# Optimization experiments

Hardware: AMD Instinct MI355X
Metric: run time of the kernel (lower is better)

Reference implementation:

```python
import jax, jax.numpy as jnp
import numpy as np
import math

B, S, D, H = 2, 2048, 1024, 16
DH = D // H
NEG = -1e9


def gelu(x):
    return 0.5 * x * (1.0 + jnp.tanh(math.sqrt(2.0 / math.pi) * (x + 0.044715 * x ** 3)))


def layernorm(x, g, b, eps=1e-6):
    # faithful to module: uses std (unbiased, N-1) and adds eps to std, not var
    mean = jnp.mean(x, axis=-1, keepdims=True)
    var = jnp.sum((x - mean) ** 2, axis=-1, keepdims=True) / (x.shape[-1] - 1)
    std = jnp.sqrt(var)
    return g * (x - mean) / (std + eps) + b


def setup_inputs() -> dict:
    key = jax.random.key(0)
    ks = jax.random.split(key, 13)
    sd = 0.02
    return {
        "x": jax.random.normal(ks[0], (B, S, D), jnp.float32),
        "w_attn": jax.random.normal(ks[1], (D, 3 * D), jnp.float32) * sd,
        "b_attn": jnp.zeros((3 * D,), jnp.float32),
        "w_aproj": jax.random.normal(ks[2], (D, D), jnp.float32) * sd,
        "b_aproj": jnp.zeros((D,), jnp.float32),
        "g1": jnp.ones((D,), jnp.float32),
        "b1": jnp.zeros((D,), jnp.float32),
        "w_fc": jax.random.normal(ks[3], (D, 4 * D), jnp.float32) * sd,
        "b_fc": jnp.zeros((4 * D,), jnp.float32),
        "w_mproj": jax.random.normal(ks[4], (4 * D, D), jnp.float32) * sd,
        "b_mproj": jnp.zeros((D,), jnp.float32),
        "g2": jnp.ones((D,), jnp.float32),
        "b2": jnp.zeros((D,), jnp.float32),
    }


def reference(x, w_attn, b_attn, w_aproj, b_aproj, g1, b1, w_fc, b_fc, w_mproj, b_mproj, g2, b2):
    # --- attention ---
    qkv = x @ w_attn + b_attn                       # [B,S,3D]
    q, k, v = jnp.split(qkv, 3, axis=2)
    q = q.reshape(B, S, H, DH).transpose(0, 2, 1, 3)  # [B,H,S,DH]
    k = k.reshape(B, S, H, DH).transpose(0, 2, 1, 3)
    v = v.reshape(B, S, H, DH).transpose(0, 2, 1, 3)
    w = jnp.einsum('bhqd,bhkd->bhqk', q, k) / math.sqrt(DH)
    mask = jnp.tril(jnp.ones((S, S), jnp.float32))[None, None]
    w = w * mask + NEG * (1.0 - mask)
    w = jax.nn.softmax(w, axis=-1)
    a = jnp.einsum('bhqk,bhkd->bhqd', w, v)         # [B,H,S,DH]
    a = a.transpose(0, 2, 1, 3).reshape(B, S, D)
    a = a @ w_aproj + b_aproj
    # --- postLN + MLP ---
    n = layernorm(x + a, g1, b1)
    h = gelu(n @ w_fc + b_fc)
    m = h @ w_mproj + b_mproj
    return layernorm(n + m, g2, b2)
```

## Files before the change

### kernel.cpp

```cpp
#include <hip/hip_runtime.h>
#include <type_traits>


typedef unsigned short u16;
typedef short s16x8 __attribute__((ext_vector_type(8)));
typedef unsigned short u16x4 __attribute__((ext_vector_type(4)));
typedef float f32x4 __attribute__((ext_vector_type(4)));
typedef float f32x16 __attribute__((ext_vector_type(16)));

__device__ __forceinline__ u16 f2b(float f) {
    union { float f; unsigned u; } x{f};
    unsigned r = x.u + 0x7FFFu + ((x.u >> 16) & 1u);
    return (u16)(r >> 16);
}

__device__ __forceinline__ float b2f(u16 v) {
    union { unsigned u; float f; } x;
    x.u = ((unsigned)v) << 16;
    return x.f;
}

__device__ __forceinline__ f32x4 mfma16(s16x8 a, s16x8 b, f32x4 c) {
    return __builtin_amdgcn_mfma_f32_16x16x32_bf16(a, b, c, 0, 0, 0);
}

__device__ __forceinline__ f32x16 mfma32(s16x8 a, s16x8 b, f32x16 c) {
    return __builtin_amdgcn_mfma_f32_32x32x16_bf16(a, b, c, 0, 0, 0);
}

__device__ __forceinline__ int cvtpk(float a, float b) {
    int r;
    asm("v_cvt_pk_bf16_f32 %0, %1, %2" : "=v"(r) : "v"(a), "v"(b));
    return r;
}

__device__ __forceinline__ void gld_lds16(const u16* g, const u16* l) {
    __builtin_amdgcn_global_load_lds(
        (const __attribute__((address_space(1))) void*)g,
        (__attribute__((address_space(3))) void*)l, 16, 0, 0);
}

__device__ __forceinline__ void hard_barrier() {
    __builtin_amdgcn_sched_barrier(0);
    __builtin_amdgcn_s_barrier();
    __builtin_amdgcn_sched_barrier(0);
}

__global__ __launch_bounds__(256) void cvt_bf16(const float* __restrict__ in,
                                                u16* __restrict__ out, int n4) {
    int i = blockIdx.x * 256 + threadIdx.x;
    if (i < n4) {
        float4 v = ((const float4*)in)[i];
        u16x4 o = {f2b(v.x), f2b(v.y), f2b(v.z), f2b(v.w)};
        ((u16x4*)out)[i] = o;
    }
}

__global__ __launch_bounds__(256) void transpose_bf16(const float* __restrict__ W,
                                                      u16* __restrict__ WT,
                                                      int K, int N) {
    __shared__ float t[32][33];
    int tx = threadIdx.x & 31, ty = threadIdx.x >> 5;
    int n0 = blockIdx.x * 32, k0 = blockIdx.y * 32;
    #pragma unroll
    for (int r = ty; r < 32; r += 8)
        t[r][tx] = W[(size_t)(k0 + r) * N + n0 + tx];
    __syncthreads();
    #pragma unroll
    for (int r = ty; r < 32; r += 8)
        WT[(size_t)(n0 + r) * K + k0 + tx] = f2b(t[tx][r]);
}

template<int BN, bool GELU, typename OT>
__global__ __launch_bounds__(256) void gemm_pl(const u16* __restrict__ A,
                                               const u16* __restrict__ BT,
                                               const float* __restrict__ bias,
                                               OT* __restrict__ C,
                                               int M, int N, int K, int ldc) {
    constexpr int NF = BN / 32;
    constexpr int BNI = BN / 32;
    constexpr int LTOT = 4 + BNI;
    __shared__ u16 As[2][128 * 64];
    __shared__ u16 Bs[2][BN * 64];

    int t = threadIdx.x;
    int w = t >> 6, l = t & 63, l16 = l & 15, lh = l >> 4;
    int wr = w >> 1, wc = w & 1;

    int nbm = M >> 7;
    int cpx = gridDim.x >> 3;
    int id = blockIdx.x;
    int id2 = (id & 7) * cpx + (id >> 3);
    size_t m0 = (size_t)(id2 % nbm) * 128;
    size_t n0 = (size_t)(id2 / nbm) * BN;

    int rowA = t >> 3;
    int gc2 = (t & 7) ^ (rowA & 7);
    const u16* Ag = A + (m0 + rowA) * (size_t)K + gc2 * 8;
    const u16* Bg = BT + (n0 + rowA) * (size_t)K + gc2 * 8;
    int wbase = w * 512;

    f32x4 acc[4][NF] = {};
    int rx = (l16 & 7) * 8;

    const s16x8* pa[2][4];
    const s16x8* pb[2][NF];
    #pragma unroll
    for (int ks = 0; ks < 2; ++ks) {
        #pragma unroll
        for (int fm = 0; fm < 4; ++fm) {
            int row = wr * 64 + fm * 16 + l16;
            int col = ((ks * 4 + lh) * 8) ^ rx;
            pa[ks][fm] = (const s16x8*)&As[0][row * 64 + col];
        }
        #pragma unroll
        for (int fn = 0; fn < NF; ++fn) {
            int row = wc * (BN / 2) + fn * 16 + l16;
            int col = ((ks * 4 + lh) * 8) ^ rx;
            pb[ks][fn] = (const s16x8*)&Bs[0][row * 64 + col];
        }
    }
    const u16* dA[4];
    const u16* dB[BNI];
    #pragma unroll
    for (int j = 0; j < 4; ++j) dA[j] = &As[0][j * 2048 + wbase];
    #pragma unroll
    for (int j = 0; j < BNI; ++j) dB[j] = &Bs[0][j * 2048 + wbase];

    #pragma unroll
    for (int j = 0; j < 4; ++j) gld_lds16(Ag + (size_t)j * 32 * K, dA[j]);
    #pragma unroll
    for (int j = 0; j < BNI; ++j) gld_lds16(Bg + (size_t)j * 32 * K, dB[j]);
    #pragma unroll
    for (int j = 0; j < 4; ++j)
        gld_lds16(Ag + 64 + (size_t)j * 32 * K, dA[j] + 8192);
    #pragma unroll
    for (int j = 0; j < BNI; ++j)
        gld_lds16(Bg + 64 + (size_t)j * 32 * K, dB[j] + BN * 64);

#define GTILE(CB, kk, LAST)                                                   \
    {                                                                         \
        if (LAST) asm volatile("s_waitcnt vmcnt(0)" ::: "memory");            \
        else      asm volatile("s_waitcnt vmcnt(%0)" :: "n"(LTOT) : "memory");\
        hard_barrier();                                                       \
        __builtin_amdgcn_s_setprio(1);                                        \
        _Pragma("unroll")                                                     \
        for (int ks = 0; ks < 2; ++ks) {                                      \
            s16x8 af[4], bf[NF];                                              \
            _Pragma("unroll")                                                 \
            for (int fm = 0; fm < 4; ++fm) af[fm] = pa[ks][fm][(CB) * 1024];  \
            _Pragma("unroll")                                                 \
            for (int fn = 0; fn < NF; ++fn) bf[fn] = pb[ks][fn][(CB) * BN * 8];\
            _Pragma("unroll")                                                 \
            for (int fm = 0; fm < 4; ++fm)                                    \
                _Pragma("unroll")                                             \
                for (int fn = 0; fn < NF; ++fn)                               \
                    acc[fm][fn] = mfma16(af[fm], bf[fn], acc[fm][fn]);        \
        }                                                                     \
        __builtin_amdgcn_s_setprio(0);                                        \
        hard_barrier();                                                       \
        if ((kk) + 128 < K) {                                                 \
            const u16* Ap = Ag + (kk) + 128;                                  \
            _Pragma("unroll")                                                 \
            for (int j = 0; j < 4; ++j)                                       \
                gld_lds16(Ap + (size_t)j * 32 * K, dA[j] + (CB) * 8192);      \
            const u16* Bp = Bg + (kk) + 128;                                  \
            _Pragma("unroll")                                                 \
            for (int j = 0; j < BNI; ++j)                                     \
                gld_lds16(Bp + (size_t)j * 32 * K, dB[j] + (CB) * (BN * 64)); \
        }                                                                     \
    }

    for (int k0 = 0; k0 < K; k0 += 128) {
        GTILE(0, k0, (k0 + 64 >= K))
        GTILE(1, k0 + 64, (k0 + 128 >= K))
    }
#undef GTILE

    #pragma unroll
    for (int fn = 0; fn < NF; ++fn) {
        size_t col = n0 + wc * (BN / 2) + fn * 16 + l16;
        float bs = bias[col];
        #pragma unroll
        for (int fm = 0; fm < 4; ++fm) {
            size_t row0 = m0 + wr * 64 + fm * 16 + lh * 4;
            #pragma unroll
            for (int i = 0; i < 4; ++i) {
                float v = acc[fm][fn][i] + bs;
                if constexpr (GELU) {
                    float x3 = v * v * v;
                    v = 0.5f * v * (1.f + tanhf(0.7978845608f * (v + 0.044715f * x3)));
                }
                if constexpr (std::is_same<OT, u16>::value)
                    C[(row0 + i) * ldc + col] = f2b(v);
                else
                    C[(row0 + i) * ldc + col] = v;
            }
        }
    }
}

__global__ __launch_bounds__(256) void attn_kernel(const u16* __restrict__ qkv,
                                                   u16* __restrict__ p0,
                                                   u16* __restrict__ p1,
                                                   u16* __restrict__ p2,
                                                   u16* __restrict__ p3,
                                                   float2* __restrict__ stats) {
    constexpr int S = 2048, D3 = 3072, Dm = 1024;
    __shared__ u16 Kl[2][64 * 64];
    __shared__ u16 Vt[2][64 * 64];

    int t = threadIdx.x;
    int w = t >> 6, l = t & 63;
    int l32 = l & 31, hi = l >> 5;
    int bid = blockIdx.x;
    int bh = bid & 31;
    int pr = (bid >> 5) & 7;
    int quar = bid >> 8;
    int b = bh >> 4, h = bh & 15;
    size_t base = (size_t)b * S * D3;

    u16* pout = quar == 0 ? p0 : (quar == 1 ? p1 : (quar == 2 ? p2 : p3));

    int rK0 = t >> 3, gK = t & 7;
    int rK1 = rK0 + 32;
    size_t koff0 = (size_t)rK0 * D3 + (size_t)((gK ^ (rK0 & 7)) * 8);
    size_t koff1 = (size_t)rK1 * D3 + (size_t)((gK ^ (rK1 & 7)) * 8);
    const u16* kbase = qkv + base + Dm + h * 64;
    const u16* vbase = qkv + base + 2 * Dm + h * 64 + w * 16;

    constexpr float cexp = 0.18033688011112042f;
    constexpr float THR = 64.0f;
    int xg = l32 & 7;

    #pragma unroll 1
    for (int ph = 0; ph < 2; ++ph) {
        int qt = ph ? (15 - pr) : pr;
        int qb = qt * 128 + w * 32;
        int nst = 2 * (qt + 1);
        int c0 = (nst * quar) >> 2;
        int c1 = (nst * (quar + 1)) >> 2;

        f32x16 O0 = {}, O1 = {};
        float m = -1e30f, lr = 0.f;

        if (c0 < c1) {
            s16x8 qf[4];
            const u16* qp = qkv + base + (size_t)(qb + l32) * D3 + h * 64 + hi * 8;
            #pragma unroll
            for (int kk = 0; kk < 4; ++kk)
                qf[kk] = *(const s16x8*)(qp + kk * 16);

            size_t kc0 = (size_t)c0 * 64 * D3;
            gld_lds16(kbase + kc0 + koff0, &Kl[0][w * 512]);
            gld_lds16(kbase + kc0 + koff1, &Kl[0][2048 + w * 512]);
            {
                const u16* vp = vbase + (size_t)(c0 * 64 + l) * D3;
                s16x8 pv0 = *(const s16x8*)vp;
                s16x8 pv1 = *(const s16x8*)(vp + 8);
                #pragma unroll
                for (int e = 0; e < 8; ++e) {
                    int d0 = w * 16 + e, d1 = w * 16 + 8 + e;
                    Vt[0][d0 * 64 + (l ^ ((d0 & 7) << 3))] = (u16)pv0[e];
                    Vt[0][d1 * 64 + (l ^ ((d1 & 7) << 3))] = (u16)pv1[e];
                }
            }
            __syncthreads();

            #pragma unroll 1
            for (int sc = c0; sc < c1; ++sc) {
                int cur = (sc - c0) & 1;
                bool pre = (sc + 1 < c1);
                s16x8 v0, v1;
                if (pre) {
                    size_t koffc = (size_t)(sc + 1) * 64 * D3;
                    gld_lds16(kbase + koffc + koff0, &Kl[cur ^ 1][w * 512]);
                    gld_lds16(kbase + koffc + koff1, &Kl[cur ^ 1][2048 + w * 512]);
                    const u16* vp = vbase + (size_t)((sc + 1) * 64 + l) * D3;
                    v0 = *(const s16x8*)vp;
                    v1 = *(const s16x8*)(vp + 8);
                }

                int kvb = sc * 64;
                int navail = ((qb - kvb) >> 5) + 1;
                if (navail > 0) {
                    if (navail > 2) navail = 2;
                    const u16* Kc = Kl[cur];
                    const u16* Vc = Vt[cur];
                    f32x16 sa0 = {}, sa1 = {};
                    #pragma unroll
                    for (int kk = 0; kk < 4; ++kk) {
                        s16x8 kf = *(const s16x8*)&Kc[l32 * 64 + (((2 * kk + hi) ^ xg) * 8)];
                        sa0 = mfma32(kf, qf[kk], sa0);
                    }
                    if (navail == 2) {
                        #pragma unroll
                        for (int kk = 0; kk < 4; ++kk) {
                            s16x8 kf = *(const s16x8*)&Kc[(32 + l32) * 64 + (((2 * kk + hi) ^ xg) * 8)];
                            sa1 = mfma32(kf, qf[kk], sa1);
                        }
                    }
                    bool diag0 = (kvb == qb);
                    bool diag1 = (kvb + 32 == qb);
                    float p[32];
                    float mx = -1e30f;
                    #pragma unroll
                    for (int reg = 0; reg < 16; ++reg) {
                        int kvloc = (reg & 3) + 8 * (reg >> 2) + 4 * hi;
                        float s0 = sa0[reg];
                        if (diag0 && kvloc > l32) s0 = -1e30f;
                        p[reg] = s0;
                        mx = fmaxf(mx, s0);
                    }
                    if (navail == 2) {
                        #pragma unroll
                        for (int reg = 0; reg < 16; ++reg) {
                            int kvloc = (reg & 3) + 8 * (reg >> 2) + 4 * hi;
                            float s1 = sa1[reg];
                            if (diag1 && kvloc > l32) s1 = -1e30f;
                            p[16 + reg] = s1;
                            mx = fmaxf(mx, s1);
                        }
                    }
                    mx = fmaxf(mx, __shfl_xor(mx, 32));
                    if (!__all(mx <= m + THR)) {
                        float mn = fmaxf(m, mx);
                        float a_ = exp2f(cexp * (m - mn));
                        m = mn;
                        #pragma unroll
                        for (int reg = 0; reg < 16; ++reg) {
                            int src = (reg & 3) + 8 * (reg >> 2) + 4 * hi;
                            float aq = __shfl(a_, src);
                            O0[reg] *= aq;
                            O1[reg] *= aq;
                        }
                        lr *= a_;
                    }
                    float cm = cexp * m;
                    float rs = 0.f;
                    #pragma unroll
                    for (int reg = 0; reg < 16; ++reg) {
                        p[reg] = exp2f(fmaf(cexp, p[reg], -cm));
                        rs += p[reg];
                    }
                    if (navail == 2) {
                        #pragma unroll
                        for (int reg = 16; reg < 32; ++reg) {
                            p[reg] = exp2f(fmaf(cexp, p[reg], -cm));
                            rs += p[reg];
                        }
                    }
                    rs += __shfl_xor(rs, 32);
                    lr += rs;

                    #pragma unroll
                    for (int c = 0; c < 4; ++c) {
                        if (c < navail * 2) {
                            int pb = (c >> 1) * 16 + (c & 1) * 8;
                            int pk01 = cvtpk(p[pb + 0], p[pb + 1]);
                            int pk23 = cvtpk(p[pb + 2], p[pb + 3]);
                            int pk45 = cvtpk(p[pb + 4], p[pb + 5]);
                            int pk67 = cvtpk(p[pb + 6], p[pb + 7]);
                            int sx01 = __shfl_xor(pk01, 32);
                            int sx23 = __shfl_xor(pk23, 32);
                            int sx45 = __shfl_xor(pk45, 32);
                            int sx67 = __shfl_xor(pk67, 32);
                            union { int i[4]; s16x8 v; } u;
                            u.i[0] = hi ? sx45 : pk01;
                            u.i[1] = hi ? sx67 : pk23;
                            u.i[2] = hi ? pk45 : sx01;
                            u.i[3] = hi ? pk67 : sx23;
                            int go = ((c * 2 + hi) ^ xg) * 8;
                            s16x8 vb0 = *(const s16x8*)&Vc[l32 * 64 + go];
                            O0 = mfma32(u.v, vb0, O0);
                            s16x8 vb1 = *(const s16x8*)&Vc[(32 + l32) * 64 + go];
                            O1 = mfma32(u.v, vb1, O1);
                        }
                    }
                }

                if (pre) {
                    #pragma unroll
                    for (int e = 0; e < 8; ++e) {
                        int d0 = w * 16 + e, d1 = w * 16 + 8 + e;
                        Vt[cur ^ 1][d0 * 64 + (l ^ ((d0 & 7) << 3))] = (u16)v0[e];
                        Vt[cur ^ 1][d1 * 64 + (l ^ ((d1 & 7) << 3))] = (u16)v1[e];
                    }
                }
                __syncthreads();
            }
        }

        size_t obase = (size_t)b * S * 1024 + h * 64;
        #pragma unroll
        for (int reg = 0; reg < 16; ++reg) {
            int src = (reg & 3) + 8 * (reg >> 2) + 4 * hi;
            size_t row = obase + (size_t)(qb + src) * 1024;
            pout[row + l32] = f2b(O0[reg]);
            pout[row + 32 + l32] = f2b(O1[reg]);
        }
        if (hi == 0) {
            float2 st; st.x = m; st.y = lr;
            stats[quar * 65536 + ((b * 2048 + qb + l32) * 16 + h)] = st;
        }
    }
}

__global__ __launch_bounds__(256) void merge_attn(u16* __restrict__ p0,
                                                  const u16* __restrict__ p1,
                                                  const u16* __restrict__ p2,
                                                  const u16* __restrict__ p3,
                                                  const float2* __restrict__ stats) {
    constexpr float cexp = 0.18033688011112042f;
    int gid = blockIdx.x * 256 + threadIdx.x;
    int rh = gid >> 2;
    int dc = (gid & 3) * 16;
    int R = rh >> 4, h = rh & 15;
    size_t addr = (size_t)R * 1024 + h * 64 + dc;

    float2 s0 = stats[rh];
    float2 s1 = stats[65536 + rh];
    float2 s2 = stats[131072 + rh];
    float2 s3 = stats[196608 + rh];
    float M = fmaxf(fmaxf(s0.x, s1.x), fmaxf(s2.x, s3.x));
    float a0 = exp2f(cexp * (s0.x - M));
    float a1 = exp2f(cexp * (s1.x - M));
    float a2 = exp2f(cexp * (s2.x - M));
    float a3 = exp2f(cexp * (s3.x - M));
    float inv = 1.f / (a0 * s0.y + a1 * s1.y + a2 * s2.y + a3 * s3.y);
    a0 *= inv; a1 *= inv; a2 *= inv; a3 *= inv;

    u16x4 o[4];
    #pragma unroll
    for (int j = 0; j < 4; ++j) {
        u16x4 q0 = *(const u16x4*)(p0 + addr + j * 4);
        u16x4 q1 = *(const u16x4*)(p1 + addr + j * 4);
        u16x4 q2 = *(const u16x4*)(p2 + addr + j * 4);
        u16x4 q3 = *(const u16x4*)(p3 + addr + j * 4);
        #pragma unroll
        for (int e = 0; e < 4; ++e)
            o[j][e] = f2b(a0 * b2f(q0[e]) + a1 * b2f(q1[e]) +
                          a2 * b2f(q2[e]) + a3 * b2f(q3[e]));
    }
    #pragma unroll
    for (int j = 0; j < 4; ++j)
        *(u16x4*)(p0 + addr + j * 4) = o[j];
}

template<bool WB>
__global__ __launch_bounds__(256) void resln(const float* __restrict__ xa,
                                             const float* __restrict__ xb2,
                                             const float* __restrict__ g,
                                             const float* __restrict__ be,
                                             float* __restrict__ outf,
                                             u16* __restrict__ outb) {
    int row = blockIdx.x;
    int t = threadIdx.x;
    size_t base = (size_t)row * 1024 + t * 4;
    float4 va = *(const float4*)(xa + base);
    float4 vb = *(const float4*)(xb2 + base);
    float v0 = va.x + vb.x, v1 = va.y + vb.y, v2 = va.z + vb.z, v3 = va.w + vb.w;
    float s1 = v0 + v1 + v2 + v3;
    float s2 = v0 * v0 + v1 * v1 + v2 * v2 + v3 * v3;
    #pragma unroll
    for (int off = 32; off >= 1; off >>= 1) {
        s1 += __shfl_down(s1, off);
        s2 += __shfl_down(s2, off);
    }
    __shared__ float r1[4], r2[4];
    if ((t & 63) == 0) { r1[t >> 6] = s1; r2[t >> 6] = s2; }
    __syncthreads();
    s1 = r1[0] + r1[1] + r1[2] + r1[3];
    s2 = r2[0] + r2[1] + r2[2] + r2[3];
    float mean = s1 * (1.f / 1024.f);
    float var = fmaxf((s2 - 1024.f * mean * mean) * (1.f / 1023.f), 0.f);
    float inv = 1.f / (sqrtf(var) + 1e-6f);
    int col = t * 4;
    float y0 = g[col + 0] * ((v0 - mean) * inv) + be[col + 0];
    float y1 = g[col + 1] * ((v1 - mean) * inv) + be[col + 1];
    float y2 = g[col + 2] * ((v2 - mean) * inv) + be[col + 2];
    float y3 = g[col + 3] * ((v3 - mean) * inv) + be[col + 3];
    float4 o = {y0, y1, y2, y3};
    *(float4*)(outf + base) = o;
    if constexpr (WB) {
        u16x4 ob = {f2b(y0), f2b(y1), f2b(y2), f2b(y3)};
        *(u16x4*)(outb + base) = ob;
    }
}

extern "C" void kernel_launch(void* const* d_in, const int* in_sizes, int n_in,
                              void* d_out, int out_size, void* d_ws, size_t ws_size,
                              hipStream_t stream) {
    (void)in_sizes; (void)n_in; (void)out_size; (void)ws_size;
    const float* x       = (const float*)d_in[0];
    const float* w_attn  = (const float*)d_in[1];
    const float* b_attn  = (const float*)d_in[2];
    const float* w_aproj = (const float*)d_in[3];
    const float* b_aproj = (const float*)d_in[4];
    const float* g1      = (const float*)d_in[5];
    const float* b1      = (const float*)d_in[6];
    const float* w_fc    = (const float*)d_in[7];
    const float* b_fc    = (const float*)d_in[8];
    const float* w_mproj = (const float*)d_in[9];
    const float* b_mproj = (const float*)d_in[10];
    const float* g2      = (const float*)d_in[11];
    const float* b2      = (const float*)d_in[12];
    float* out = (float*)d_out;

    constexpr int M = 4096;
    constexpr int D = 1024;

    char* ws = (char*)d_ws;
    u16*   slotA = (u16*)ws;
    char*  pB    = ws + (32u << 20);
    char*  pC    = ws + (40u << 20);
    char*  pD    = ws + (48u << 20);
    char*  pE    = ws + (64u << 20);

    u16*   xb    = (u16*)pB;
    u16*   wT    = (u16*)pC;
    u16*   qkv   = slotA;
    u16*   part0 = (u16*)pB;
    u16*   part1 = (u16*)pC;
    u16*   part2 = (u16*)pD;
    u16*   part3 = (u16*)(pD + (8u << 20));
    float2* stat = (float2*)pE;
    u16*   abuf  = (u16*)pB;
    float* aout  = (float*)pD;
    float* nbuf  = (float*)pE;
    u16*   nb    = (u16*)pB;
    u16*   h     = slotA;
    float* mout  = (float*)pD;

    dim3 blk(256);

    cvt_bf16<<<dim3(4096), blk, 0, stream>>>(x, xb, M * D / 4);

    transpose_bf16<<<dim3(3072 / 32, 1024 / 32), blk, 0, stream>>>(w_attn, wT, 1024, 3072);
    gemm_pl<128, false, u16><<<dim3((M / 128) * (3072 / 128)), blk, 0, stream>>>(
        xb, wT, b_attn, qkv, M, 3072, 1024, 3072);

    attn_kernel<<<dim3(1024), blk, 0, stream>>>(qkv, part0, part1, part2, part3, stat);
    merge_attn<<<dim3(1024), blk, 0, stream>>>(part0, part1, part2, part3, stat);

    transpose_bf16<<<dim3(1024 / 32, 1024 / 32), blk, 0, stream>>>(w_aproj, wT, 1024, 1024);
    gemm_pl<64, false, float><<<dim3((M / 128) * (1024 / 64)), blk, 0, stream>>>(
        abuf, wT, b_aproj, aout, M, 1024, 1024, 1024);

    resln<true><<<dim3(M), blk, 0, stream>>>(x, aout, g1, b1, nbuf, nb);

    transpose_bf16<<<dim3(4096 / 32, 1024 / 32), blk, 0, stream>>>(w_fc, wT, 1024, 4096);
    gemm_pl<128, true, u16><<<dim3((M / 128) * (4096 / 128)), blk, 0, stream>>>(
        nb, wT, b_fc, h, M, 4096, 1024, 4096);

    transpose_bf16<<<dim3(1024 / 32, 4096 / 32), blk, 0, stream>>>(w_mproj, wT, 4096, 1024);
    gemm_pl<64, false, float><<<dim3((M / 128) * (1024 / 64)), blk, 0, stream>>>(
        h, wT, b_mproj, mout, M, 1024, 4096, 1024);

    resln<false><<<dim3(M), blk, 0, stream>>>(nbuf, mout, g2, b2, out, nullptr);
}
```

Measured before the change: 286.3 us.

## Use 512-thread GEMM blocks with 2x4 wave grid

Doubles the GEMM workgroup to 8 waves, arranged 2x4, so each wave computes a narrower 64 x BN/4 sub-tile. The global-to-LDS copy is redistributed across 512 threads, and LDS fragment addresses are now computed inline instead of from precomputed pointer arrays. The aim is more resident waves to hide memory and MFMA latency. The cost is less register-level reuse per wave, more LDS reads per MFMA, and heavier block barriers.

```diff
diff --git a/kernel.cpp b/kernel.cpp
--- a/kernel.cpp
+++ b/kernel.cpp
@@ -72,20 +72,20 @@
 }
 
 template<int BN, bool GELU, typename OT>
-__global__ __launch_bounds__(256) void gemm_pl(const u16* __restrict__ A,
+__global__ __launch_bounds__(512) void gemm_pl(const u16* __restrict__ A,
                                                const u16* __restrict__ BT,
                                                const float* __restrict__ bias,
                                                OT* __restrict__ C,
                                                int M, int N, int K, int ldc) {
-    constexpr int NF = BN / 32;
-    constexpr int BNI = BN / 32;
-    constexpr int LTOT = 4 + BNI;
+    constexpr int NF = BN / 64;
+    constexpr int BNI = BN / 64;
+    constexpr int LTOT = 2 + BNI;
     __shared__ u16 As[2][128 * 64];
     __shared__ u16 Bs[2][BN * 64];
 
     int t = threadIdx.x;
     int w = t >> 6, l = t & 63, l16 = l & 15, lh = l >> 4;
-    int wr = w >> 1, wc = w & 1;
+    int wr = w >> 2, wc = w & 3;
 
     int nbm = M >> 7;
     int cpx = gridDim.x >> 3;
@@ -98,45 +98,23 @@
     int gc2 = (t & 7) ^ (rowA & 7);
     const u16* Ag = A + (m0 + rowA) * (size_t)K + gc2 * 8;
     const u16* Bg = BT + (n0 + rowA) * (size_t)K + gc2 * 8;
-    int wbase = w * 512;
+    int wb = w * 512;
 
     f32x4 acc[4][NF] = {};
     int rx = (l16 & 7) * 8;
 
-    const s16x8* pa[2][4];
-    const s16x8* pb[2][NF];
-    #pragma unroll
-    for (int ks = 0; ks < 2; ++ks) {
-        #pragma unroll
-        for (int fm = 0; fm < 4; ++fm) {
-            int row = wr * 64 + fm * 16 + l16;
-            int col = ((ks * 4 + lh) * 8) ^ rx;
-            pa[ks][fm] = (const s16x8*)&As[0][row * 64 + col];
-        }
-        #pragma unroll
-        for (int fn = 0; fn < NF; ++fn) {
-            int row = wc * (BN / 2) + fn * 16 + l16;
-            int col = ((ks * 4 + lh) * 8) ^ rx;
-            pb[ks][fn] = (const s16x8*)&Bs[0][row * 64 + col];
-        }
-    }
-    const u16* dA[4];
-    const u16* dB[BNI];
-    #pragma unroll
-    for (int j = 0; j < 4; ++j) dA[j] = &As[0][j * 2048 + wbase];
-    #pragma unroll
-    for (int j = 0; j < BNI; ++j) dB[j] = &Bs[0][j * 2048 + wbase];
-
-    #pragma unroll
-    for (int j = 0; j < 4; ++j) gld_lds16(Ag + (size_t)j * 32 * K, dA[j]);
-    #pragma unroll
-    for (int j = 0; j < BNI; ++j) gld_lds16(Bg + (size_t)j * 32 * K, dB[j]);
-    #pragma unroll
-    for (int j = 0; j < 4; ++j)
-        gld_lds16(Ag + 64 + (size_t)j * 32 * K, dA[j] + 8192);
+    #pragma unroll
+    for (int j = 0; j < 2; ++j)
+        gld_lds16(Ag + (size_t)j * 64 * K, &As[0][j * 4096 + wb]);
     #pragma unroll
     for (int j = 0; j < BNI; ++j)
-        gld_lds16(Bg + 64 + (size_t)j * 32 * K, dB[j] + BN * 64);
+        gld_lds16(Bg + (size_t)j * 64 * K, &Bs[0][j * 4096 + wb]);
+    #pragma unroll
+    for (int j = 0; j < 2; ++j)
+        gld_lds16(Ag + 64 + (size_t)j * 64 * K, &As[1][j * 4096 + wb]);
+    #pragma unroll
+    for (int j = 0; j < BNI; ++j)
+        gld_lds16(Bg + 64 + (size_t)j * 64 * K, &Bs[1][j * 4096 + wb]);
 
 #define GTILE(CB, kk, LAST)                                                   \
     {                                                                         \
@@ -148,9 +126,17 @@
         for (int ks = 0; ks < 2; ++ks) {                                      \
             s16x8 af[4], bf[NF];                                              \
             _Pragma("unroll")                                                 \
-            for (int fm = 0; fm < 4; ++fm) af[fm] = pa[ks][fm][(CB) * 1024];  \
+            for (int fm = 0; fm < 4; ++fm) {                                  \
+                int row = wr * 64 + fm * 16 + l16;                            \
+                int col = ((ks * 4 + lh) * 8) ^ rx;                           \
+                af[fm] = *(const s16x8*)&As[CB][row * 64 + col];              \
+            }                                                                 \
             _Pragma("unroll")                                                 \
-            for (int fn = 0; fn < NF; ++fn) bf[fn] = pb[ks][fn][(CB) * BN * 8];\
+            for (int fn = 0; fn < NF; ++fn) {                                 \
+                int row = wc * (BN / 4) + fn * 16 + l16;                      \
+                int col = ((ks * 4 + lh) * 8) ^ rx;                           \
+                bf[fn] = *(const s16x8*)&Bs[CB][row * 64 + col];              \
+            }                                                                 \
             _Pragma("unroll")                                                 \
             for (int fm = 0; fm < 4; ++fm)                                    \
                 _Pragma("unroll")                                             \
@@ -162,12 +148,12 @@
         if ((kk) + 128 < K) {                                                 \
             const u16* Ap = Ag + (kk) + 128;                                  \
             _Pragma("unroll")                                                 \
-            for (int j = 0; j < 4; ++j)                                       \
-                gld_lds16(Ap + (size_t)j * 32 * K, dA[j] + (CB) * 8192);      \
+            for (int j = 0; j < 2; ++j)                                       \
+                gld_lds16(Ap + (size_t)j * 64 * K, &As[CB][j * 4096 + wb]);   \
             const u16* Bp = Bg + (kk) + 128;                                  \
             _Pragma("unroll")                                                 \
             for (int j = 0; j < BNI; ++j)                                     \
-                gld_lds16(Bp + (size_t)j * 32 * K, dB[j] + (CB) * (BN * 64)); \
+                gld_lds16(Bp + (size_t)j * 64 * K, &Bs[CB][j * 4096 + wb]);   \
         }                                                                     \
     }
 
@@ -179,7 +165,7 @@
 
     #pragma unroll
     for (int fn = 0; fn < NF; ++fn) {
-        size_t col = n0 + wc * (BN / 2) + fn * 16 + l16;
+        size_t col = n0 + wc * (BN / 4) + fn * 16 + l16;
         float bs = bias[col];
         #pragma unroll
         for (int fm = 0; fm < 4; ++fm) {
@@ -533,28 +519,29 @@
     float* mout  = (float*)pD;
 
     dim3 blk(256);
+    dim3 blk512(512);
 
     cvt_bf16<<<dim3(4096), blk, 0, stream>>>(x, xb, M * D / 4);
 
     transpose_bf16<<<dim3(3072 / 32, 1024 / 32), blk, 0, stream>>>(w_attn, wT, 1024, 3072);
-    gemm_pl<128, false, u16><<<dim3((M / 128) * (3072 / 128)), blk, 0, stream>>>(
+    gemm_pl<128, false, u16><<<dim3((M / 128) * (3072 / 128)), blk512, 0, stream>>>(
         xb, wT, b_attn, qkv, M, 3072, 1024, 3072);
 
     attn_kernel<<<dim3(1024), blk, 0, stream>>>(qkv, part0, part1, part2, part3, stat);
     merge_attn<<<dim3(1024), blk, 0, stream>>>(part0, part1, part2, part3, stat);
 
     transpose_bf16<<<dim3(1024 / 32, 1024 / 32), blk, 0, stream>>>(w_aproj, wT, 1024, 1024);
-    gemm_pl<64, false, float><<<dim3((M / 128) * (1024 / 64)), blk, 0, stream>>>(
+    gemm_pl<64, false, float><<<dim3((M / 128) * (1024 / 64)), blk512, 0, stream>>>(
         abuf, wT, b_aproj, aout, M, 1024, 1024, 1024);
 
     resln<true><<<dim3(M), blk, 0, stream>>>(x, aout, g1, b1, nbuf, nb);
 
     transpose_bf16<<<dim3(4096 / 32, 1024 / 32), blk, 0, stream>>>(w_fc, wT, 1024, 4096);
-    gemm_pl<128, true, u16><<<dim3((M / 128) * (4096 / 128)), blk, 0, stream>>>(
+    gemm_pl<128, true, u16><<<dim3((M / 128) * (4096 / 128)), blk512, 0, stream>>>(
         nb, wT, b_fc, h, M, 4096, 1024, 4096);
 
     transpose_bf16<<<dim3(1024 / 32, 4096 / 32), blk, 0, stream>>>(w_mproj, wT, 4096, 1024);
-    gemm_pl<64, false, float><<<dim3((M / 128) * (1024 / 64)), blk, 0, stream>>>(
+    gemm_pl<64, false, float><<<dim3((M / 128) * (1024 / 64)), blk512, 0, stream>>>(
         h, wT, b_mproj, mout, M, 1024, 4096, 1024);
 
     resln<false><<<dim3(M), blk, 0, stream>>>(nbuf, mout, g2, b2, out, nullptr);
```

New measurement: 269.3 us. -5.9%, faster.
